# Performance work log

Hardware: AMD Instinct MI355X
Metric: run time of the kernel (lower is better)

## Reference

```python
import jax, jax.numpy as jnp
import numpy as np

N, F, T, E = 20000, 128, 4, 640000
TBL = 10002  # oscillator lookup: indices 0..10001 (clamped inputs map to 10001)
EPS = 1e-5


def setup_inputs() -> dict:
    key = jax.random.key(0)
    ks = jax.random.split(key, 12)
    rn = lambda k, shp, s: (jax.random.normal(k, shp, dtype=jnp.float32) * s)
    return {
        "x": rn(ks[0], (N, F), 1.0),
        "osc_table": jax.random.uniform(ks[1], (TBL,), dtype=jnp.float32),
        "edge_index": jax.random.randint(ks[2], (2, E), 0, N, dtype=jnp.int32),
        "edge_type": jax.random.randint(ks[3], (E,), 0, T, dtype=jnp.int32),
        "w_ih": rn(ks[4], (4 * F, F), 0.05),
        "w_hh": rn(ks[5], (4 * F, F), 0.05),
        "b_ih": jnp.zeros((4 * F,), jnp.float32),
        "b_hh": jnp.zeros((4 * F,), jnp.float32),
        "conv1_w": rn(ks[6], (T, 2 * F, F), 0.001),
        "conv1_b": jnp.zeros((2 * F,), jnp.float32),
        "conv2_w": rn(ks[7], (T, F, 2 * F), 0.001),
        "conv2_b": jnp.zeros((F,), jnp.float32),
        "lin1_w": rn(ks[8], (2 * F, F), 0.05),
        "lin1_b": jnp.zeros((2 * F,), jnp.float32),
        "lin2_w": rn(ks[9], (F, 2 * F), 0.05),
        "lin2_b": jnp.zeros((F,), jnp.float32),
        "bn1_g": jnp.ones((2 * F,), jnp.float32),
        "bn1_b": jnp.zeros((2 * F,), jnp.float32),
        "bn2_g": jnp.ones((F,), jnp.float32),
        "bn2_b": jnp.zeros((F,), jnp.float32),
    }


def _oscillator(x, table):
    # clamp out-of-range inputs to 0.5001 -> index 10001
    xi = jnp.where((x < -0.5) | (x > 0.5), jnp.float32(0.5001), x)
    idx = jnp.floor((xi + 0.5) * 10000.0).astype(jnp.int32)
    vals = table[idx]
    # where table value is 0, fall back to Sig'(original input) = sigmoid(x) (s=1)
    return jnp.where(vals == 0, jax.nn.sigmoid(x), vals)


def _ec_conv(x, W, b, src, dst, etype):
    # per-edge-type scatter-MAX aggregation, vectorized via composite segment ids
    msgs = x[src]                                  # [E, Cin]
    seg = dst * T + etype                          # [E]
    agg = jax.ops.segment_max(msgs, seg, num_segments=N * T)  # [N*T, Cin]
    agg = jnp.where(jnp.isfinite(agg), agg, 0.0)   # empty segments (-inf) -> 0 (PyG zero-fill)
    agg = agg.reshape(N, T, -1)
    # sum_t linear(agg_t, W_t, b) ; bias is added once per edge type in the torch loop
    return jnp.einsum("ntc,toc->no", agg, W) + T * b


def _batchnorm(x, gamma, beta):
    mu = jnp.mean(x, axis=0)
    var = jnp.mean((x - mu) ** 2, axis=0)          # biased variance (training mode)
    return (x - mu) * jax.lax.rsqrt(var + EPS) * gamma + beta


def reference(x, osc_table, edge_index, edge_type, w_ih, w_hh, b_ih, b_hh,
              conv1_w, conv1_b, conv2_w, conv2_b, lin1_w, lin1_b, lin2_w, lin2_b,
              bn1_g, bn1_b, bn2_g, bn2_b):
    src, dst = edge_index[0], edge_index[1]
    h = _oscillator(x, osc_table)
    # LSTM over a length-1 sequence (unsqueeze(0), batch_first=False) with zero state:
    gates = h @ w_ih.T + b_ih + b_hh               # h0=0 so w_hh contributes nothing
    i, f, g, o = jnp.split(gates, 4, axis=-1)
    c = jax.nn.sigmoid(i) * jnp.tanh(g)
    h = jax.nn.sigmoid(o) * jnp.tanh(c)
    h = h @ lin1_w.T + lin1_b + _ec_conv(h, conv1_w, conv1_b, src, dst, edge_type)
    h = jax.nn.relu(_batchnorm(h, bn1_g, bn1_b))
    h = h @ lin2_w.T + lin2_b + _ec_conv(h, conv2_w, conv2_b, src, dst, edge_type)
    h = _batchnorm(h, bn2_g, bn2_b)
    return jax.nn.sigmoid(h - 10.0)
```

## Files before the change

kernel.cpp:

```cpp
#include <hip/hip_runtime.h>
#include <math.h>

#define NN 20000
#define NE 640000
#define TT 4
#define FF 128
#define FF2 256
#define NSEG (NN*TT)
#define MP 20096
#define NBUCK 157
#define EPSBN 1e-5f

typedef short bf16x8 __attribute__((ext_vector_type(8)));
typedef float f32x4  __attribute__((ext_vector_type(4)));
typedef unsigned short us2 __attribute__((ext_vector_type(2)));

__device__ __forceinline__ float sigf(float x){ return 1.0f/(1.0f+expf(-x)); }

__device__ __forceinline__ unsigned short f2bf(float x){
  union { float f; unsigned u; } v; v.f = x;
  unsigned r = v.u + 0x7FFF + ((v.u >> 16) & 1);
  return (unsigned short)(r >> 16);
}
__device__ __forceinline__ float bf2f(unsigned short u){
  union { float f; unsigned u; } v; v.u = ((unsigned)u) << 16; return v.f;
}

__device__ __forceinline__ unsigned char f2f8(float x){
  union{float f; unsigned u;} v; v.f = x;
  unsigned s = (v.u >> 24) & 0x80u;
  unsigned a = v.u & 0x7FFFFFFFu;
  if(a > 0x43E00000u) a = 0x43E00000u;
  union{unsigned u; float f;} w; w.u = a;
  float ax = w.f;
  if(ax < 0.015625f){
    int q = (int)rintf(ax * 512.0f);
    return (unsigned char)(s | (unsigned)q);
  }
  unsigned rb = a & 0xFFFFFu;
  unsigned base = a >> 20;
  unsigned r = base + (((rb > 0x80000u) || (rb == 0x80000u && (base & 1u))) ? 1u : 0u);
  unsigned e = r >> 3, m3 = r & 7u;
  int fe = (int)e - 120;
  if(fe >= 16) return (unsigned char)(s | 0x7Eu);
  return (unsigned char)(s | ((unsigned)fe << 3) | m3);
}
__device__ __forceinline__ unsigned char fold8(unsigned char b){
  return (unsigned char)(b ^ ((b & 0x80u) ? 0xFFu : 0x80u));
}
__device__ __forceinline__ unsigned short key8tobf(unsigned char k){
  unsigned char b = (unsigned char)(k ^ ((k & 0x80u) ? 0x80u : 0xFFu));
  unsigned s = ((unsigned)b & 0x80u) << 24;
  unsigned e = ((unsigned)b >> 3) & 0xFu;
  unsigned m = (unsigned)b & 7u;
  union{unsigned u; float f;} v;
  if(e == 0){ v.f = (float)m * 0.001953125f; v.u |= s; }
  else v.u = s | ((e + 120u) << 23) | (m << 20);
  return (unsigned short)(v.u >> 16);
}
__device__ __forceinline__ void acc8(unsigned v, unsigned &me, unsigned &mo){
  union U{unsigned u; us2 v;};
  U a, b, r;
  a.u = __builtin_amdgcn_perm(v, 0u, 0x0C060C04u);
  b.u = me; r.v = __builtin_elementwise_max(a.v, b.v); me = r.u;
  a.u = __builtin_amdgcn_perm(v, 0u, 0x0C070C05u);
  b.u = mo; r.v = __builtin_elementwise_max(a.v, b.v); mo = r.u;
}
__device__ __forceinline__ unsigned maxsplit(unsigned a, unsigned b){
  union U{unsigned u; us2 v;};
  U x, y, r; x.u = a; y.u = b;
  r.v = __builtin_elementwise_max(x.v, y.v);
  return r.u;
}

#define PB0 147456
#define PB1 (PB0 + 229376)
#define PB2 (PB1 + 229376)
__global__ __launch_bounds__(256)
void k_prep(const float* __restrict__ w_ih, const float* __restrict__ lin1_w,
            const float* __restrict__ conv1_w, const float* __restrict__ lin2_w,
            const float* __restrict__ conv2_w,
            const float* __restrict__ bih, const float* __restrict__ bhh,
            const float* __restrict__ l1b, const float* __restrict__ c1b,
            const float* __restrict__ l2b, const float* __restrict__ c2b,
            unsigned short* __restrict__ Bp0, unsigned short* __restrict__ Bp1,
            unsigned short* __restrict__ Bp2,
            float* __restrict__ bias0, float* __restrict__ bias1, float* __restrict__ bias2,
            int* __restrict__ gbcnt, int* __restrict__ gcursor,
            float* __restrict__ bnsum1, float* __restrict__ bnsum2){
  int gi = blockIdx.x*256 + threadIdx.x;
  if(gi < PB0){
    int k = gi/384, o = gi - k*384;
    int grow = (o < 128) ? o : o + 128;
    int reg = k >> 7, c = k & 127;
    float w = w_ih[(size_t)grow*128 + c];
    unsigned short hu = f2bf(w);
    Bp0[((size_t)(k >> 3)*384 + o)*8 + (k & 7)] = (reg == 1) ? f2bf(w - bf2f(hu)) : hu;
  } else if(gi < PB1){
    int i = gi - PB0; int k = i >> 8, o = i & 255;
    int reg = k >> 7;
    unsigned short val;
    if(reg < 3){
      float w = lin1_w[(size_t)o*128 + (k & 127)];
      unsigned short hu = f2bf(w);
      val = (reg == 1) ? f2bf(w - bf2f(hu)) : hu;
    } else {
      int kk = k - 384; int t = kk >> 7; int c = kk & 127;
      val = f2bf(conv1_w[((size_t)t*256 + o)*128 + c]);
    }
    Bp1[((size_t)(k >> 3)*256 + o)*8 + (k & 7)] = val;
  } else if(gi < PB2){
    int i = gi - PB1; int k = i >> 7, o = i & 127;
    int reg = k >> 8;
    unsigned short val;
    if(reg < 3){
      float w = lin2_w[(size_t)o*256 + (k & 255)];
      unsigned short hu = f2bf(w);
      val = (reg == 1) ? f2bf(w - bf2f(hu)) : hu;
    } else {
      int kk = k - 768; int t = kk >> 8; int c = kk & 255;
      val = f2bf(conv2_w[((size_t)t*128 + o)*256 + c]);
    }
    Bp2[((size_t)(k >> 3)*128 + o)*8 + (k & 7)] = val;
  } else {
    int t = gi - PB2;
    if(t < 384){ int grow = (t < 128) ? t : t + 128; bias0[t] = bih[grow] + bhh[grow]; }
    else if(t < 640){ int c = t - 384; bias1[c] = l1b[c] + 4.0f*c1b[c]; }
    else if(t < 768){ int c = t - 640; bias2[c] = l2b[c] + 4.0f*c2b[c]; }
    else if(t < 1280){ bnsum1[t - 768] = 0.0f; }
    else if(t < 1536){ bnsum2[t - 1280] = 0.0f; }
    else if(t < 1536 + NBUCK){ gbcnt[t - 1536] = 0; }
    else if(t < 1536 + 2*NBUCK){ gcursor[t - 1536 - NBUCK] = 0; }
  }
}

__global__ void k_osc_pack(const float* __restrict__ x, const float* __restrict__ tbl,
                           unsigned short* __restrict__ A0){
  int i = blockIdx.x*256 + threadIdx.x;
  if(i >= NN*FF) return;
  int n = i >> 7, j = i & 127;
  float xv = x[i];
  float xi = (xv < -0.5f || xv > 0.5f) ? 0.5001f : xv;
  int idx = (int)floorf((xi + 0.5f) * 10000.0f);
  float tv = tbl[idx];
  float hv = (tv == 0.0f) ? sigf(xv) : tv;
  unsigned short hu = f2bf(hv);
  unsigned short lu = f2bf(hv - bf2f(hu));
  unsigned short* r = A0 + (size_t)n*256;
  r[j] = hu; r[128+j] = lu;
}

template<int C, int COUT, int SPLITS, int AK>
__global__ __launch_bounds__(256)
void k_gemm(const unsigned short* __restrict__ A, const unsigned short* __restrict__ Bp,
            float* __restrict__ out){
  int w  = threadIdx.x >> 6;
  int l  = threadIdx.x & 63;
  int wr = w >> 1, wc = w & 1;
  int lr = l & 15, lg = l >> 4;
  int n0 = blockIdx.x*128 + wr*64;
  int c0 = blockIdx.y*128 + wc*64;
  constexpr int Q = (AK + C)/SPLITS;
  int zq0 = blockIdx.z*Q, zq1 = zq0 + Q;
  int kb = (zq0 <= 2*C) ? (zq0 >> 1) : (zq0 - C);
  int ke = (zq1 <= 2*C) ? (zq1 >> 1) : (zq1 - C);
  const size_t abase = (size_t)(n0 + lr)*AK + lg*8;
  const size_t bstep = (size_t)COUT*8;
  const unsigned short* bcolp = Bp + (size_t)(c0 + lr)*8 + lg*bstep;
  f32x4 acc[4][4] = {};
  int kde = ke < C ? ke : C;
  for(int ak = kb; ak < kde; ak += 32){
    bf16x8 a[4];
    #pragma unroll
    for(int r = 0; r < 4; ++r) a[r] = *(const bf16x8*)(A + abase + (size_t)r*16*AK + ak);
    const unsigned short* p1 = bcolp + (size_t)(ak >> 3)*bstep;
    const unsigned short* p2 = bcolp + (size_t)((C + ak) >> 3)*bstep;
    #pragma unroll
    for(int j = 0; j < 4; ++j){
      bf16x8 b1 = *(const bf16x8*)(p1 + j*128);
      bf16x8 b2 = *(const bf16x8*)(p2 + j*128);
      #pragma unroll
      for(int r = 0; r < 4; ++r){
        acc[r][j] = __builtin_amdgcn_mfma_f32_16x16x32_bf16(a[r], b1, acc[r][j], 0, 0, 0);
        acc[r][j] = __builtin_amdgcn_mfma_f32_16x16x32_bf16(a[r], b2, acc[r][j], 0, 0, 0);
      }
    }
  }
  int ks = kb > C ? kb : C;
  for(int ak = ks; ak < ke; ak += 32){
    bf16x8 a[4];
    #pragma unroll
    for(int r = 0; r < 4; ++r) a[r] = *(const bf16x8*)(A + abase + (size_t)r*16*AK + ak);
    const unsigned short* p = bcolp + (size_t)((C + ak) >> 3)*bstep;
    #pragma unroll
    for(int j = 0; j < 4; ++j){
      bf16x8 b = *(const bf16x8*)(p + j*128);
      #pragma unroll
      for(int r = 0; r < 4; ++r)
        acc[r][j] = __builtin_amdgcn_mfma_f32_16x16x32_bf16(a[r], b, acc[r][j], 0, 0, 0);
    }
  }
  float* o = out + (size_t)blockIdx.z*NN*COUT;
  #pragma unroll
  for(int r = 0; r < 4; ++r){
    int nb = n0 + r*16 + lg*4;
    #pragma unroll
    for(int j = 0; j < 4; ++j){
      int oc = c0 + j*16 + lr;
      #pragma unroll
      for(int q = 0; q < 4; ++q){
        int n = nb + q;
        if(n < NN) o[(size_t)n*COUT + oc] = acc[r][j][q];
      }
    }
  }
}

template<int COUT, int SPLITS>
__global__ __launch_bounds__(COUT)
void k_reduce(const float* __restrict__ P, const float* __restrict__ bias,
              float* __restrict__ h, float* __restrict__ sums){
  int c = threadIdx.x;
  float bs = bias[c];
  float s = 0.0f, s2 = 0.0f;
  for(int n = blockIdx.x; n < NN; n += gridDim.x){
    float v = bs;
    #pragma unroll
    for(int z = 0; z < SPLITS; ++z) v += P[(size_t)z*NN*COUT + (size_t)n*COUT + c];
    h[(size_t)n*COUT + c] = v;
    s += v; s2 += v*v;
  }
  atomicAdd(&sums[c], s);
  atomicAdd(&sums[COUT + c], s2);
}

__global__ void k_act(const float* __restrict__ gates, const float* __restrict__ bias0,
                      unsigned short* __restrict__ A1, unsigned char* __restrict__ h1k8){
  int i = blockIdx.x*256 + threadIdx.x;
  if(i >= NN*FF) return;
  int n = i >> 7, j = i & 127;
  const float* g = gates + (size_t)n*384;
  float ig = g[j]       + bias0[j];
  float gg = g[128 + j] + bias0[128 + j];
  float og = g[256 + j] + bias0[256 + j];
  float c  = sigf(ig) * tanhf(gg);
  float hv = sigf(og) * tanhf(c);
  unsigned short hu = f2bf(hv);
  unsigned short lu = f2bf(hv - bf2f(hu));
  unsigned short* r = A1 + (size_t)n*768;
  r[j] = hu; r[128 + j] = lu;
  h1k8[i] = fold8(f2f8(hv));
}

__global__ void k_bcount(const int* __restrict__ dst, int* __restrict__ gbcnt){
  __shared__ int h[NBUCK];
  for(int i = threadIdx.x; i < NBUCK; i += 256) h[i] = 0;
  __syncthreads();
  int e0 = blockIdx.x*2048;
  #pragma unroll
  for(int k = 0; k < 8; ++k){
    int e = e0 + threadIdx.x + k*256;
    if(e < NE) atomicAdd(&h[dst[e] >> 7], 1);
  }
  __syncthreads();
  for(int i = threadIdx.x; i < NBUCK; i += 256) if(h[i]) atomicAdd(&gbcnt[i], h[i]);
}
__global__ void k_bscan(const int* __restrict__ gbcnt, int* __restrict__ gbase,
                        int* __restrict__ excl){
  if(threadIdx.x == 0){
    int s = 0;
    for(int i = 0; i < NBUCK; ++i){ gbase[i] = s; s += gbcnt[i]; }
    excl[NSEG] = s;
  }
}
__global__ __launch_bounds__(512)
void k_binscat(const int* __restrict__ src, const int* __restrict__ dst,
               const int* __restrict__ et, const int* __restrict__ gbase,
               int* __restrict__ gcursor, unsigned* __restrict__ gstage){
  __shared__ unsigned stage[4096];
  __shared__ unsigned char stgb[4096];
  __shared__ int lcnt[NBUCK], lexc[NBUCK], lcur[NBUCK], gofs[NBUCK];
  int tid = threadIdx.x;
  for(int i = tid; i < NBUCK; i += 512) lcnt[i] = 0;
  __syncthreads();
  int e0 = blockIdx.x*4096;
  int b_[8]; unsigned v_[8];
  #pragma unroll
  for(int k = 0; k < 8; ++k){
    int e = e0 + tid + k*512;
    if(e < NE){
      int d = dst[e]; int b = d >> 7;
      b_[k] = b;
      v_[k] = ((unsigned)((((d & 127) << 2) | et[e])) << 16) | (unsigned)src[e];
      atomicAdd(&lcnt[b], 1);
    } else b_[k] = -1;
  }
  __syncthreads();
  if(tid == 0){
    int s = 0;
    for(int i = 0; i < NBUCK; ++i){ lexc[i] = s; s += lcnt[i]; }
  }
  __syncthreads();
  if(tid < NBUCK){
    lcur[tid] = lexc[tid];
    if(lcnt[tid]) gofs[tid] = atomicAdd(&gcursor[tid], lcnt[tid]);
  }
  __syncthreads();
  #pragma unroll
  for(int k = 0; k < 8; ++k){
    if(b_[k] >= 0){
      int p = atomicAdd(&lcur[b_[k]], 1);
      stage[p] = v_[k]; stgb[p] = (unsigned char)b_[k];
    }
  }
  __syncthreads();
  int ne = NE - e0; if(ne > 4096) ne = 4096;
  for(int i = tid; i < ne; i += 512){
    int b = stgb[i];
    gstage[gbase[b] + gofs[b] + (i - lexc[b])] = stage[i];
  }
}
__global__ __launch_bounds__(512)
void k_fine(const unsigned* __restrict__ gstage, const int* __restrict__ gbcnt,
            const int* __restrict__ gbase, int* __restrict__ excl,
            unsigned short* __restrict__ elist){
  __shared__ int cnt[512], scn[512], cur[512];
  int t = threadIdx.x, bk = blockIdx.x;
  cnt[t] = 0;
  __syncthreads();
  int gB = gbase[bk], cE = gbcnt[bk];
  for(int i = t; i < cE; i += 512) atomicAdd(&cnt[gstage[gB + i] >> 16], 1);
  __syncthreads();
  scn[t] = cnt[t]; __syncthreads();
  for(int off = 1; off < 512; off <<= 1){
    int add = (t >= off) ? scn[t - off] : 0;
    __syncthreads();
    scn[t] += add;
    __syncthreads();
  }
  int ex = scn[t] - cnt[t];
  cur[t] = ex;
  int s = bk*512 + t;
  if(s < NSEG) excl[s] = gB + ex;
  __syncthreads();
  for(int i = t; i < cE; i += 512){
    unsigned v = gstage[gB + i];
    int p = atomicAdd(&cur[v >> 16], 1);
    elist[gB + p] = (unsigned short)(v & 0xFFFFu);
  }
}

template<int C, int AK>
__global__ __launch_bounds__(256)
void k_agg8(const unsigned char* __restrict__ keys, const unsigned short* __restrict__ elist,
            const int* __restrict__ excl, unsigned short* __restrict__ A){
  constexpr int NW = C/128;
  __shared__ unsigned short slut[256];
  if(threadIdx.x < 256) slut[threadIdx.x] = key8tobf((unsigned char)threadIdx.x);
  __syncthreads();
  int seg  = blockIdx.x*4 + (threadIdx.x >> 6);
  int l = threadIdx.x & 63, half = l >> 5, cl = l & 31;
  int start = excl[seg];
  int cnt   = excl[seg + 1] - start;
  const unsigned char* kp = keys + cl*(NW*4);
  unsigned me0 = 0, mo0 = 0, me1 = 0, mo1 = 0;
  for(int bb = 0; bb < cnt; bb += 64){
    int m = cnt - bb; if(m > 64) m = 64;
    int ee = (int)elist[start + bb + l];
    int k = 0;
    for(; k + 8 <= m; k += 8){
      int e0 = __shfl(ee, k + half);
      int e1 = __shfl(ee, k + 2 + half);
      int e2 = __shfl(ee, k + 4 + half);
      int e3 = __shfl(ee, k + 6 + half);
      if constexpr(NW == 1){
        unsigned v0 = *(const unsigned*)(kp + (size_t)e0*C);
        unsigned v1 = *(const unsigned*)(kp + (size_t)e1*C);
        unsigned v2 = *(const unsigned*)(kp + (size_t)e2*C);
        unsigned v3 = *(const unsigned*)(kp + (size_t)e3*C);
        acc8(v0, me0, mo0); acc8(v1, me0, mo0);
        acc8(v2, me0, mo0); acc8(v3, me0, mo0);
      } else {
        uint2 v0 = *(const uint2*)(kp + (size_t)e0*C);
        uint2 v1 = *(const uint2*)(kp + (size_t)e1*C);
        uint2 v2 = *(const uint2*)(kp + (size_t)e2*C);
        uint2 v3 = *(const uint2*)(kp + (size_t)e3*C);
        acc8(v0.x, me0, mo0); acc8(v0.y, me1, mo1);
        acc8(v1.x, me0, mo0); acc8(v1.y, me1, mo1);
        acc8(v2.x, me0, mo0); acc8(v2.y, me1, mo1);
        acc8(v3.x, me0, mo0); acc8(v3.y, me1, mo1);
      }
    }
    for(; k + 2 <= m; k += 2){
      int e = __shfl(ee, k + half);
      if constexpr(NW == 1){
        acc8(*(const unsigned*)(kp + (size_t)e*C), me0, mo0);
      } else {
        uint2 v = *(const uint2*)(kp + (size_t)e*C);
        acc8(v.x, me0, mo0); acc8(v.y, me1, mo1);
      }
    }
    if(k < m){
      int e = __shfl(ee, k);
      if(half == 0){
        if constexpr(NW == 1){
          acc8(*(const unsigned*)(kp + (size_t)e*C), me0, mo0);
        } else {
          uint2 v = *(const uint2*)(kp + (size_t)e*C);
          acc8(v.x, me0, mo0); acc8(v.y, me1, mo1);
        }
      }
    }
  }
  me0 = maxsplit(me0, (unsigned)__shfl_xor((int)me0, 32));
  mo0 = maxsplit(mo0, (unsigned)__shfl_xor((int)mo0, 32));
  if constexpr(NW == 2){
    me1 = maxsplit(me1, (unsigned)__shfl_xor((int)me1, 32));
    mo1 = maxsplit(mo1, (unsigned)__shfl_xor((int)mo1, 32));
  }
  if(half == 0){
    int n = seg >> 2, t = seg & 3;
    unsigned short* op = A + (size_t)n*AK + 2*C + t*C + cl*(NW*4);
    if constexpr(NW == 1){
      typedef unsigned short u4 __attribute__((ext_vector_type(4)));
      u4 o;
      o[0] = cnt ? slut[me0 & 0xFF] : (unsigned short)0;
      o[1] = cnt ? slut[mo0 & 0xFF] : (unsigned short)0;
      o[2] = cnt ? slut[(me0 >> 16) & 0xFF] : (unsigned short)0;
      o[3] = cnt ? slut[(mo0 >> 16) & 0xFF] : (unsigned short)0;
      *(u4*)op = o;
    } else {
      typedef unsigned short u8v __attribute__((ext_vector_type(8)));
      u8v o;
      o[0] = cnt ? slut[me0 & 0xFF] : (unsigned short)0;
      o[1] = cnt ? slut[mo0 & 0xFF] : (unsigned short)0;
      o[2] = cnt ? slut[(me0 >> 16) & 0xFF] : (unsigned short)0;
      o[3] = cnt ? slut[(mo0 >> 16) & 0xFF] : (unsigned short)0;
      o[4] = cnt ? slut[me1 & 0xFF] : (unsigned short)0;
      o[5] = cnt ? slut[mo1 & 0xFF] : (unsigned short)0;
      o[6] = cnt ? slut[(me1 >> 16) & 0xFF] : (unsigned short)0;
      o[7] = cnt ? slut[(mo1 >> 16) & 0xFF] : (unsigned short)0;
      *(u8v*)op = o;
    }
  }
}

__global__ void k_bnrp(const float* __restrict__ h2, const float* __restrict__ sums,
                       const float* __restrict__ g, const float* __restrict__ bb,
                       unsigned short* __restrict__ A2, unsigned char* __restrict__ h2k8){
  int i = blockIdx.x*256 + threadIdx.x;
  if(i >= NN*FF2) return;
  int n = i >> 8, c = i & 255;
  float mean = sums[c] * (1.0f/NN);
  float var  = sums[256 + c] * (1.0f/NN) - mean*mean;
  float scale = g[c] / sqrtf(var + EPSBN);
  float shift = bb[c] - mean*scale;
  float v = fmaxf(h2[i]*scale + shift, 0.0f);
  unsigned short hu = f2bf(v);
  unsigned short lu = f2bf(v - bf2f(hu));
  unsigned short* r = A2 + (size_t)n*1536;
  r[c] = hu; r[256 + c] = lu;
  h2k8[i] = fold8(f2f8(v));
}

__global__ void k_bnsig(float* __restrict__ h, const float* __restrict__ sums,
                        const float* __restrict__ g, const float* __restrict__ bb){
  int i = blockIdx.x*256 + threadIdx.x;
  if(i >= NN*FF) return;
  int c = i & 127;
  float mean = sums[c] * (1.0f/NN);
  float var  = sums[128 + c] * (1.0f/NN) - mean*mean;
  float scale = g[c] / sqrtf(var + EPSBN);
  float shift = bb[c] - mean*scale;
  float v = h[i]*scale + shift - 10.0f;
  h[i] = 1.0f/(1.0f + expf(-v));
}

extern "C" void kernel_launch(void* const* d_in, const int* in_sizes, int n_in,
                              void* d_out, int out_size, void* d_ws, size_t ws_size,
                              hipStream_t stream){
  (void)in_sizes; (void)n_in; (void)out_size; (void)ws_size;
  const float* x       = (const float*)d_in[0];
  const float* tbl     = (const float*)d_in[1];
  const int*   eidx    = (const int*)  d_in[2];
  const int*   etype   = (const int*)  d_in[3];
  const float* w_ih    = (const float*)d_in[4];
  const float* b_ih    = (const float*)d_in[6];
  const float* b_hh    = (const float*)d_in[7];
  const float* conv1_w = (const float*)d_in[8];
  const float* conv1_b = (const float*)d_in[9];
  const float* conv2_w = (const float*)d_in[10];
  const float* conv2_b = (const float*)d_in[11];
  const float* lin1_w  = (const float*)d_in[12];
  const float* lin1_b  = (const float*)d_in[13];
  const float* lin2_w  = (const float*)d_in[14];
  const float* lin2_b  = (const float*)d_in[15];
  const float* bn1_g   = (const float*)d_in[16];
  const float* bn1_b   = (const float*)d_in[17];
  const float* bn2_g   = (const float*)d_in[18];
  const float* bn2_b   = (const float*)d_in[19];
  float* out = (float*)d_out;

  char* base = (char*)d_ws;
  size_t off = 0;
  auto alloc = [&](size_t bytes){ char* p = base + off; off = (off + bytes + 255) & ~(size_t)255; return p; };

  unsigned short* A0 = (unsigned short*)alloc((size_t)MP * 256 * 2);
  unsigned short* A1 = (unsigned short*)alloc((size_t)MP * 768 * 2);
  unsigned short* A2 = (unsigned short*)alloc((size_t)MP * 1536 * 2);
  float* h2raw = (float*)alloc((size_t)NN * 256 * 4);
  unsigned char* h1k8 = (unsigned char*)alloc((size_t)NN * 128);
  unsigned char* h2k8 = (unsigned char*)alloc((size_t)NN * 256);
  unsigned short* Bp0 = (unsigned short*)alloc((size_t)384 * 384 * 2);
  unsigned short* Bp1 = (unsigned short*)alloc((size_t)896 * 256 * 2);
  unsigned short* Bp2 = (unsigned short*)alloc((size_t)1792 * 128 * 2);
  float* bias0 = (float*)alloc(384 * 4);
  float* bias1 = (float*)alloc(256 * 4);
  float* bias2 = (float*)alloc(128 * 4);
  int* excl    = (int*)alloc((NSEG + 1) * 4);
  float* bnsum1 = (float*)alloc(512 * 4);
  float* bnsum2 = (float*)alloc(256 * 4);
  int* gbcnt   = (int*)alloc(NBUCK * 4);
  int* gbase   = (int*)alloc(NBUCK * 4);
  int* gcursor = (int*)alloc(NBUCK * 4);
  unsigned* gstage = (unsigned*)alloc((size_t)NE * 4);
  unsigned short* elist = (unsigned short*)alloc((size_t)NE * 2 + 256);

  float* gates = (float*)A2;
  float* P1    = (float*)A2;
  float* P2    = (float*)A0;

  const int* src = eidx;
  const int* dst = eidx + NE;

  k_prep<<<(PB2 + 1850 + 255)/256, 256, 0, stream>>>(
      w_ih, lin1_w, conv1_w, lin2_w, conv2_w,
      b_ih, b_hh, lin1_b, conv1_b, lin2_b, conv2_b,
      Bp0, Bp1, Bp2, bias0, bias1, bias2, gbcnt, gcursor, bnsum1, bnsum2);

  k_osc_pack<<<(NN*FF + 255)/256, 256, 0, stream>>>(x, tbl, A0);

  k_bcount<<<(NE + 2047)/2048, 256, 0, stream>>>(dst, gbcnt);
  k_bscan<<<1, 64, 0, stream>>>(gbcnt, gbase, excl);
  k_binscat<<<(NE + 4095)/4096, 512, 0, stream>>>(src, dst, etype, gbase, gcursor, gstage);
  k_fine<<<NBUCK, 512, 0, stream>>>(gstage, gbcnt, gbase, excl, elist);

  k_gemm<128, 384, 1, 256><<<dim3(157, 3, 1), 256, 0, stream>>>(A0, Bp0, gates);
  k_act<<<(NN*FF + 255)/256, 256, 0, stream>>>(gates, bias0, A1, h1k8);

  k_agg8<128, 768><<<NSEG/4, 256, 0, stream>>>(h1k8, elist, excl, A1);
  k_gemm<128, 256, 2, 768><<<dim3(157, 2, 2), 256, 0, stream>>>(A1, Bp1, P1);
  k_reduce<256, 2><<<256, 256, 0, stream>>>(P1, bias1, h2raw, bnsum1);
  k_bnrp<<<(NN*FF2 + 255)/256, 256, 0, stream>>>(h2raw, bnsum1, bn1_g, bn1_b, A2, h2k8);

  k_agg8<256, 1536><<<NSEG/4, 256, 0, stream>>>(h2k8, elist, excl, A2);
  k_gemm<256, 128, 4, 1536><<<dim3(157, 1, 4), 256, 0, stream>>>(A2, Bp2, P2);
  k_reduce<128, 4><<<256, 128, 0, stream>>>(P2, bias2, out, bnsum2);
  k_bnsig<<<(NN*FF + 255)/256, 256, 0, stream>>>(out, bnsum2, bn2_g, bn2_b);
}
```

Before: 277.5 us.

## Fold bucket scan into count kernel, parallelize local scan, widen agg8 lanes

The single-thread bucket scan kernel is removed. The last block of k_bcount, detected with a completion counter, now does a parallel prefix scan over the bucket counts. k_binscat's serial per-block scan becomes a Hillis-Steele scan in shared memory. k_agg8 now handles 16 segments per 1024-thread block, with each lane covering more channels through wider loads and four edge groups per wave, which cuts launch and serial-loop overhead. Clamping out-of-range edge indices to the last valid one keeps max-aggregation correct, though it adds redundant loads for segments with few edges.

Measured after the change: 289.4 us. 4.3% more time.

```diff
diff --git a/kernel.cpp b/kernel.cpp
--- a/kernel.cpp
+++ b/kernel.cpp
@@ -14,6 +14,7 @@
 typedef short bf16x8 __attribute__((ext_vector_type(8)));
 typedef float f32x4  __attribute__((ext_vector_type(4)));
 typedef unsigned short us2 __attribute__((ext_vector_type(2)));
+typedef unsigned short us8 __attribute__((ext_vector_type(8)));
 
 __device__ __forceinline__ float sigf(float x){ return 1.0f/(1.0f+expf(-x)); }
 
@@ -87,7 +88,8 @@
             unsigned short* __restrict__ Bp2,
             float* __restrict__ bias0, float* __restrict__ bias1, float* __restrict__ bias2,
             int* __restrict__ gbcnt, int* __restrict__ gcursor,
-            float* __restrict__ bnsum1, float* __restrict__ bnsum2){
+            float* __restrict__ bnsum1, float* __restrict__ bnsum2,
+            int* __restrict__ done){
   int gi = blockIdx.x*256 + threadIdx.x;
   if(gi < PB0){
     int k = gi/384, o = gi - k*384;
@@ -131,6 +133,7 @@
     else if(t < 1536){ bnsum2[t - 1280] = 0.0f; }
     else if(t < 1536 + NBUCK){ gbcnt[t - 1536] = 0; }
     else if(t < 1536 + 2*NBUCK){ gcursor[t - 1536 - NBUCK] = 0; }
+    else if(t == 1536 + 2*NBUCK){ done[0] = 0; }
   }
 }
 
@@ -252,8 +255,12 @@
   h1k8[i] = fold8(f2f8(hv));
 }
 
-__global__ void k_bcount(const int* __restrict__ dst, int* __restrict__ gbcnt){
+__global__ __launch_bounds__(256)
+void k_bcount(const int* __restrict__ dst, int* __restrict__ gbcnt,
+              int* __restrict__ gbase, int* __restrict__ excl, int* __restrict__ done){
   __shared__ int h[NBUCK];
+  __shared__ int s[256];
+  __shared__ int sdone;
   for(int i = threadIdx.x; i < NBUCK; i += 256) h[i] = 0;
   __syncthreads();
   int e0 = blockIdx.x*2048;
@@ -264,13 +271,22 @@
   }
   __syncthreads();
   for(int i = threadIdx.x; i < NBUCK; i += 256) if(h[i]) atomicAdd(&gbcnt[i], h[i]);
-}
-__global__ void k_bscan(const int* __restrict__ gbcnt, int* __restrict__ gbase,
-                        int* __restrict__ excl){
-  if(threadIdx.x == 0){
-    int s = 0;
-    for(int i = 0; i < NBUCK; ++i){ gbase[i] = s; s += gbcnt[i]; }
-    excl[NSEG] = s;
+  __threadfence();
+  __syncthreads();
+  if(threadIdx.x == 0) sdone = (atomicAdd(done, 1) == (int)gridDim.x - 1);
+  __syncthreads();
+  if(sdone){
+    int t = threadIdx.x;
+    int v = (t < NBUCK) ? atomicAdd(&gbcnt[t], 0) : 0;
+    s[t] = v; __syncthreads();
+    for(int off = 1; off < 256; off <<= 1){
+      int add = (t >= off) ? s[t - off] : 0;
+      __syncthreads();
+      s[t] += add;
+      __syncthreads();
+    }
+    if(t < NBUCK) gbase[t] = s[t] - v;
+    if(t == 255) excl[NSEG] = s[255];
   }
 }
 __global__ __launch_bounds__(512)
@@ -280,6 +296,7 @@
   __shared__ unsigned stage[4096];
   __shared__ unsigned char stgb[4096];
   __shared__ int lcnt[NBUCK], lexc[NBUCK], lcur[NBUCK], gofs[NBUCK];
+  __shared__ int s2[256];
   int tid = threadIdx.x;
   for(int i = tid; i < NBUCK; i += 512) lcnt[i] = 0;
   __syncthreads();
@@ -296,10 +313,15 @@
     } else b_[k] = -1;
   }
   __syncthreads();
-  if(tid == 0){
-    int s = 0;
-    for(int i = 0; i < NBUCK; ++i){ lexc[i] = s; s += lcnt[i]; }
-  }
+  if(tid < 256) s2[tid] = (tid < NBUCK) ? lcnt[tid] : 0;
+  __syncthreads();
+  for(int off = 1; off < 256; off <<= 1){
+    int add = (tid < 256 && tid >= off) ? s2[tid - off] : 0;
+    __syncthreads();
+    if(tid < 256) s2[tid] += add;
+    __syncthreads();
+  }
+  if(tid < NBUCK) lexc[tid] = s2[tid] - lcnt[tid];
   __syncthreads();
   if(tid < NBUCK){
     lcur[tid] = lexc[tid];
@@ -351,96 +373,76 @@
 }
 
 template<int C, int AK>
-__global__ __launch_bounds__(256)
+__global__ __launch_bounds__(1024)
 void k_agg8(const unsigned char* __restrict__ keys, const unsigned short* __restrict__ elist,
             const int* __restrict__ excl, unsigned short* __restrict__ A){
-  constexpr int NW = C/128;
+  constexpr int NQ = C/64;
   __shared__ unsigned short slut[256];
   if(threadIdx.x < 256) slut[threadIdx.x] = key8tobf((unsigned char)threadIdx.x);
   __syncthreads();
-  int seg  = blockIdx.x*4 + (threadIdx.x >> 6);
-  int l = threadIdx.x & 63, half = l >> 5, cl = l & 31;
+  int seg = blockIdx.x*16 + (threadIdx.x >> 6);
+  int l = threadIdx.x & 63, q = l >> 4, cl = l & 15;
   int start = excl[seg];
   int cnt   = excl[seg + 1] - start;
-  const unsigned char* kp = keys + cl*(NW*4);
-  unsigned me0 = 0, mo0 = 0, me1 = 0, mo1 = 0;
-  for(int bb = 0; bb < cnt; bb += 64){
-    int m = cnt - bb; if(m > 64) m = 64;
-    int ee = (int)elist[start + bb + l];
-    int k = 0;
-    for(; k + 8 <= m; k += 8){
-      int e0 = __shfl(ee, k + half);
-      int e1 = __shfl(ee, k + 2 + half);
-      int e2 = __shfl(ee, k + 4 + half);
-      int e3 = __shfl(ee, k + 6 + half);
-      if constexpr(NW == 1){
-        unsigned v0 = *(const unsigned*)(kp + (size_t)e0*C);
-        unsigned v1 = *(const unsigned*)(kp + (size_t)e1*C);
-        unsigned v2 = *(const unsigned*)(kp + (size_t)e2*C);
-        unsigned v3 = *(const unsigned*)(kp + (size_t)e3*C);
-        acc8(v0, me0, mo0); acc8(v1, me0, mo0);
-        acc8(v2, me0, mo0); acc8(v3, me0, mo0);
-      } else {
-        uint2 v0 = *(const uint2*)(kp + (size_t)e0*C);
-        uint2 v1 = *(const uint2*)(kp + (size_t)e1*C);
-        uint2 v2 = *(const uint2*)(kp + (size_t)e2*C);
-        uint2 v3 = *(const uint2*)(kp + (size_t)e3*C);
-        acc8(v0.x, me0, mo0); acc8(v0.y, me1, mo1);
-        acc8(v1.x, me0, mo0); acc8(v1.y, me1, mo1);
-        acc8(v2.x, me0, mo0); acc8(v2.y, me1, mo1);
-        acc8(v3.x, me0, mo0); acc8(v3.y, me1, mo1);
-      }
-    }
-    for(; k + 2 <= m; k += 2){
-      int e = __shfl(ee, k + half);
-      if constexpr(NW == 1){
-        acc8(*(const unsigned*)(kp + (size_t)e*C), me0, mo0);
-      } else {
-        uint2 v = *(const uint2*)(kp + (size_t)e*C);
-        acc8(v.x, me0, mo0); acc8(v.y, me1, mo1);
-      }
-    }
-    if(k < m){
-      int e = __shfl(ee, k);
-      if(half == 0){
-        if constexpr(NW == 1){
-          acc8(*(const unsigned*)(kp + (size_t)e*C), me0, mo0);
+  const unsigned char* kp = keys + cl*(NQ*4);
+  unsigned me[NQ], mo[NQ];
+  #pragma unroll
+  for(int j = 0; j < NQ; ++j){ me[j] = 0; mo[j] = 0; }
+  if(cnt > 0){
+    for(int bb = 0; bb < cnt; bb += 64){
+      int m = cnt - bb; if(m > 64) m = 64;
+      int wi = bb + l; if(wi >= cnt) wi = cnt - 1;
+      int ee = (int)elist[start + wi];
+      for(int k = 0; k < m; k += 8){
+        int i0 = k + q;     if(i0 >= m) i0 = m - 1;
+        int i1 = k + 4 + q; if(i1 >= m) i1 = m - 1;
+        int e0 = __shfl(ee, i0);
+        int e1 = __shfl(ee, i1);
+        if constexpr(NQ == 2){
+          uint2 v0 = *(const uint2*)(kp + (size_t)e0*C);
+          uint2 v1 = *(const uint2*)(kp + (size_t)e1*C);
+          acc8(v0.x, me[0], mo[0]); acc8(v0.y, me[1], mo[1]);
+          acc8(v1.x, me[0], mo[0]); acc8(v1.y, me[1], mo[1]);
         } else {
-          uint2 v = *(const uint2*)(kp + (size_t)e*C);
-          acc8(v.x, me0, mo0); acc8(v.y, me1, mo1);
+          uint4 v0 = *(const uint4*)(kp + (size_t)e0*C);
+          uint4 v1 = *(const uint4*)(kp + (size_t)e1*C);
+          acc8(v0.x, me[0], mo[0]); acc8(v0.y, me[1], mo[1]);
+          acc8(v0.z, me[2], mo[2]); acc8(v0.w, me[3], mo[3]);
+          acc8(v1.x, me[0], mo[0]); acc8(v1.y, me[1], mo[1]);
+          acc8(v1.z, me[2], mo[2]); acc8(v1.w, me[3], mo[3]);
         }
       }
     }
   }
-  me0 = maxsplit(me0, (unsigned)__shfl_xor((int)me0, 32));
-  mo0 = maxsplit(mo0, (unsigned)__shfl_xor((int)mo0, 32));
-  if constexpr(NW == 2){
-    me1 = maxsplit(me1, (unsigned)__shfl_xor((int)me1, 32));
-    mo1 = maxsplit(mo1, (unsigned)__shfl_xor((int)mo1, 32));
-  }
-  if(half == 0){
+  #pragma unroll
+  for(int j = 0; j < NQ; ++j){
+    me[j] = maxsplit(me[j], (unsigned)__shfl_xor((int)me[j], 16));
+    mo[j] = maxsplit(mo[j], (unsigned)__shfl_xor((int)mo[j], 16));
+    me[j] = maxsplit(me[j], (unsigned)__shfl_xor((int)me[j], 32));
+    mo[j] = maxsplit(mo[j], (unsigned)__shfl_xor((int)mo[j], 32));
+  }
+  if(l < 16){
     int n = seg >> 2, t = seg & 3;
-    unsigned short* op = A + (size_t)n*AK + 2*C + t*C + cl*(NW*4);
-    if constexpr(NW == 1){
-      typedef unsigned short u4 __attribute__((ext_vector_type(4)));
-      u4 o;
-      o[0] = cnt ? slut[me0 & 0xFF] : (unsigned short)0;
-      o[1] = cnt ? slut[mo0 & 0xFF] : (unsigned short)0;
-      o[2] = cnt ? slut[(me0 >> 16) & 0xFF] : (unsigned short)0;
-      o[3] = cnt ? slut[(mo0 >> 16) & 0xFF] : (unsigned short)0;
-      *(u4*)op = o;
+    unsigned short* op = A + (size_t)n*AK + 2*C + t*C + cl*(NQ*4);
+    if(cnt == 0){
+      us8 z = {};
+      *(us8*)op = z;
+      if constexpr(NQ == 4) *(us8*)(op + 8) = z;
     } else {
-      typedef unsigned short u8v __attribute__((ext_vector_type(8)));
-      u8v o;
-      o[0] = cnt ? slut[me0 & 0xFF] : (unsigned short)0;
-      o[1] = cnt ? slut[mo0 & 0xFF] : (unsigned short)0;
-      o[2] = cnt ? slut[(me0 >> 16) & 0xFF] : (unsigned short)0;
-      o[3] = cnt ? slut[(mo0 >> 16) & 0xFF] : (unsigned short)0;
-      o[4] = cnt ? slut[me1 & 0xFF] : (unsigned short)0;
-      o[5] = cnt ? slut[mo1 & 0xFF] : (unsigned short)0;
-      o[6] = cnt ? slut[(me1 >> 16) & 0xFF] : (unsigned short)0;
-      o[7] = cnt ? slut[(mo1 >> 16) & 0xFF] : (unsigned short)0;
-      *(u8v*)op = o;
+      us8 o0;
+      o0[0] = slut[me[0] & 0xFF];  o0[1] = slut[mo[0] & 0xFF];
+      o0[2] = slut[(me[0] >> 16) & 0xFF]; o0[3] = slut[(mo[0] >> 16) & 0xFF];
+      o0[4] = slut[me[1] & 0xFF];  o0[5] = slut[mo[1] & 0xFF];
+      o0[6] = slut[(me[1] >> 16) & 0xFF]; o0[7] = slut[(mo[1] >> 16) & 0xFF];
+      *(us8*)op = o0;
+      if constexpr(NQ == 4){
+        us8 o1;
+        o1[0] = slut[me[2] & 0xFF];  o1[1] = slut[mo[2] & 0xFF];
+        o1[2] = slut[(me[2] >> 16) & 0xFF]; o1[3] = slut[(mo[2] >> 16) & 0xFF];
+        o1[4] = slut[me[3] & 0xFF];  o1[5] = slut[mo[3] & 0xFF];
+        o1[6] = slut[(me[3] >> 16) & 0xFF]; o1[7] = slut[(mo[3] >> 16) & 0xFF];
+        *(us8*)(op + 8) = o1;
+      }
     }
   }
 }
@@ -523,6 +525,7 @@
   int* gbcnt   = (int*)alloc(NBUCK * 4);
   int* gbase   = (int*)alloc(NBUCK * 4);
   int* gcursor = (int*)alloc(NBUCK * 4);
+  int* done    = (int*)alloc(4);
   unsigned* gstage = (unsigned*)alloc((size_t)NE * 4);
   unsigned short* elist = (unsigned short*)alloc((size_t)NE * 2 + 256);
 
@@ -533,27 +536,26 @@
   const int* src = eidx;
   const int* dst = eidx + NE;
 
-  k_prep<<<(PB2 + 1850 + 255)/256, 256, 0, stream>>>(
+  k_prep<<<(PB2 + 2048 + 255)/256, 256, 0, stream>>>(
       w_ih, lin1_w, conv1_w, lin2_w, conv2_w,
       b_ih, b_hh, lin1_b, conv1_b, lin2_b, conv2_b,
-      Bp0, Bp1, Bp2, bias0, bias1, bias2, gbcnt, gcursor, bnsum1, bnsum2);
+      Bp0, Bp1, Bp2, bias0, bias1, bias2, gbcnt, gcursor, bnsum1, bnsum2, done);
 
   k_osc_pack<<<(NN*FF + 255)/256, 256, 0, stream>>>(x, tbl, A0);
 
-  k_bcount<<<(NE + 2047)/2048, 256, 0, stream>>>(dst, gbcnt);
-  k_bscan<<<1, 64, 0, stream>>>(gbcnt, gbase, excl);
+  k_bcount<<<(NE + 2047)/2048, 256, 0, stream>>>(dst, gbcnt, gbase, excl, done);
   k_binscat<<<(NE + 4095)/4096, 512, 0, stream>>>(src, dst, etype, gbase, gcursor, gstage);
   k_fine<<<NBUCK, 512, 0, stream>>>(gstage, gbcnt, gbase, excl, elist);
 
   k_gemm<128, 384, 1, 256><<<dim3(157, 3, 1), 256, 0, stream>>>(A0, Bp0, gates);
   k_act<<<(NN*FF + 255)/256, 256, 0, stream>>>(gates, bias0, A1, h1k8);
 
-  k_agg8<128, 768><<<NSEG/4, 256, 0, stream>>>(h1k8, elist, excl, A1);
+  k_agg8<128, 768><<<NSEG/16, 1024, 0, stream>>>(h1k8, elist, excl, A1);
   k_gemm<128, 256, 2, 768><<<dim3(157, 2, 2), 256, 0, stream>>>(A1, Bp1, P1);
   k_reduce<256, 2><<<256, 256, 0, stream>>>(P1, bias1, h2raw, bnsum1);
   k_bnrp<<<(NN*FF2 + 255)/256, 256, 0, stream>>>(h2raw, bnsum1, bn1_g, bn1_b, A2, h2k8);
 
-  k_agg8<256, 1536><<<NSEG/4, 256, 0, stream>>>(h2k8, elist, excl, A2);
+  k_agg8<256, 1536><<<NSEG/16, 1024, 0, stream>>>(h2k8, elist, excl, A2);
   k_gemm<256, 128, 4, 1536><<<dim3(157, 1, 4), 256, 0, stream>>>(A2, Bp2, P2);
   k_reduce<128, 4><<<256, 128, 0, stream>>>(P2, bias2, out, bnsum2);
   k_bnsig<<<(NN*FF + 255)/256, 256, 0, stream>>>(out, bnsum2, bn2_g, bn2_b);
```
